# Kernel tuning notes

Hardware: AMD Instinct MI355X
Metric: run time of the kernel (lower is better)

Reference implementation:

```python
import jax, jax.numpy as jnp
import numpy as np

M, K, N, G = 4096, 4096, 4096, 128


def setup_inputs() -> dict:
    key = jax.random.key(0)
    k1, k2, k3 = jax.random.split(key, 3)
    a = jax.random.normal(k1, (M, K), dtype=jnp.float16)
    # 4-bit unsigned quantized weights, values in [0, 16)
    w_q = jax.random.randint(k2, (K, N), 0, 16, dtype=jnp.int32)
    # group-wise scales: one per (k-group, n); small magnitude keeps fp16 output in range
    scale = jax.random.uniform(k3, (K // G, N), dtype=jnp.float16, minval=0.001, maxval=0.02)
    return {"a": a, "w_q": w_q, "scale": scale, "group_size": G}


def reference(a, w_q, scale, group_size):
    # Dequantize: w[k, n] = w_q[k, n] * scale[k // group_size, n]
    scale_full = jnp.repeat(scale, group_size, axis=0)  # [K, N]
    w = w_q.astype(a.dtype) * scale_full                # fp16 dequantized weight
    out = jnp.matmul(a, w, preferred_element_type=jnp.float32)
    return out.astype(jnp.float16)
```

## Files before the change

kernel.cpp:

```cpp
#include <hip/hip_runtime.h>
#include <hip/hip_fp16.h>

#define MDIM 4096
#define NDIM 4096
#define KDIM 4096
#define NT 256
#define WBLK 4096

typedef _Float16 f16x8 __attribute__((ext_vector_type(8)));
typedef float f32x4 __attribute__((ext_vector_type(4)));
typedef unsigned int u32;
typedef unsigned short u16;

__device__ inline __half2 as_half2(u32 u) { return __builtin_bit_cast(__half2, u); }
__device__ inline u32 as_u32(__half2 h) { return __builtin_bit_cast(u32, h); }
__device__ inline u32 pkrtz(float a, float b) {
  return __builtin_bit_cast(u32, __builtin_amdgcn_cvt_pkrtz(a, b));
}

__device__ inline void load16_to_lds(const void* g, void* l) {
  __builtin_amdgcn_global_load_lds(
      (__attribute__((address_space(1))) const u32*)g,
      (__attribute__((address_space(3))) u32*)l,
      16, 0, 0);
}

template <int VM>
__device__ __forceinline__ void wait_vmcnt() {
  if constexpr (VM == 8)
    asm volatile("s_waitcnt vmcnt(8)" ::: "memory");
  else if constexpr (VM == 4)
    asm volatile("s_waitcnt vmcnt(4)" ::: "memory");
  else
    asm volatile("s_waitcnt vmcnt(0)" ::: "memory");
}

__global__ __launch_bounds__(NT) void prep(const float* __restrict__ A,
                                           _Float16* __restrict__ A16,
                                           const int* __restrict__ Wq,
                                           const float* __restrict__ Sc,
                                           _Float16* __restrict__ Wt) {
  __shared__ u32 Lt[64 * 33];
  const int tid = threadIdx.x;

  if (blockIdx.x >= WBLK) {
    const size_t b = blockIdx.x - WBLK;
    const size_t base = (b * NT + tid) * 8;
    const float4 f0 = *(const float4*)(A + base);
    const float4 f1 = *(const float4*)(A + base + 4);
    u32 pk[4];
    pk[0] = pkrtz(f0.x, f0.y);
    pk[1] = pkrtz(f0.z, f0.w);
    pk[2] = pkrtz(f1.x, f1.y);
    pk[3] = pkrtz(f1.z, f1.w);
    *(uint4*)(A16 + base) = *(const uint4*)pk;
    return;
  }

  const int n0 = (blockIdx.x & 63) * 64;
  const int k0 = (blockIdx.x >> 6) * 64;
  const int g = k0 >> 7;

#pragma unroll
  for (int r = 0; r < 2; ++r) {
    const int idx = r * 256 + tid;
    const int kp = idx >> 4;
    const int col4 = (idx & 15) * 4;
    const int4 va = *(const int4*)(Wq + (size_t)(k0 + 2 * kp) * NDIM + n0 + col4);
    const int4 vb = *(const int4*)(Wq + (size_t)(k0 + 2 * kp + 1) * NDIM + n0 + col4);
    const float4 s = *(const float4*)(Sc + (size_t)g * NDIM + n0 + col4);
    const float sf[4] = {s.x, s.y, s.z, s.w};
    const int av[4] = {va.x, va.y, va.z, va.w};
    const int bv[4] = {vb.x, vb.y, vb.z, vb.w};
#pragma unroll
    for (int i = 0; i < 4; ++i) {
      const __half hs = __float2half(sf[i]);
      const __half2 s2 = __half2half2(hs);
      const __half2 nb = __half2half2(__hmul(hs, __float2half(-1024.0f)));
      const u32 u = (u32)av[i] | ((u32)bv[i] << 16) | 0x64006400u;
      Lt[(size_t)(col4 + i) * 33 + kp] = as_u32(__hfma2(as_half2(u), s2, nb));
    }
  }
  __syncthreads();

#pragma unroll
  for (int r = 0; r < 2; ++r) {
    const int idx = r * 256 + tid;
    const int n = idx >> 3;
    const int k2c = (idx & 7) * 4;
    u32 v[4];
#pragma unroll
    for (int j = 0; j < 4; ++j) v[j] = Lt[(size_t)n * 33 + k2c + j];
    *(uint4*)(Wt + (size_t)(n0 + n) * KDIM + k0 + k2c * 2) = *(const uint4*)v;
  }
}

__global__ __launch_bounds__(512, 2) void gemm_f16(const _Float16* __restrict__ A16,
                                                   const _Float16* __restrict__ Wt,
                                                   float* __restrict__ C) {
  __shared__ __align__(16) _Float16 As[4 * 256 * 32];
  __shared__ __align__(16) _Float16 Bs[4 * 256 * 32];

  const int tid = threadIdx.x;
  const int bx = blockIdx.x & 15;
  const int by = blockIdx.x >> 4;
  const int m_base = by * 256;
  const int n_base = bx * 256;

  const int wave = tid >> 6;
  const int lane = tid & 63;
  const int l15 = lane & 15;
  const int quad = lane >> 4;
  const int mq = wave >> 2;
  const int nq = wave & 3;
  const int gq = (l15 >> 1) & 3;
  const int pchunk = quad ^ gq;

  f32x4 acc[8][4];
#pragma unroll
  for (int i = 0; i < 8; ++i)
#pragma unroll
    for (int j = 0; j < 4; ++j) acc[i][j] = (f32x4)0.0f;

  auto stage = [&](int p) {
    const int T = p >> 1;
    const int h = p & 1;
    const int s = p & 3;
    const size_t kof = (size_t)T * 64 + (size_t)h * 32;
#pragma unroll
    for (int L = 0; L < 2; ++L) {
      const int cc = L * 512 + tid;
      const int row = cc >> 2;
      const int lch = (cc & 3) ^ ((row >> 1) & 3);
      load16_to_lds(A16 + (size_t)(m_base + row) * KDIM + kof + lch * 8,
                    (char*)As + (size_t)s * 16384 + (size_t)cc * 16);
    }
#pragma unroll
    for (int L = 0; L < 2; ++L) {
      const int cc = L * 512 + tid;
      const int row = cc >> 2;
      const int lch = (cc & 3) ^ ((row >> 1) & 3);
      load16_to_lds(Wt + (size_t)(n_base + row) * KDIM + kof + lch * 8,
                    (char*)Bs + (size_t)s * 16384 + (size_t)cc * 16);
    }
  };

  auto phase_body = [&](int p, bool dostage) {
    __builtin_amdgcn_s_barrier();
    asm volatile("" ::: "memory");
    const int s = p & 3;
    const _Float16* Ab = (const _Float16*)((const char*)As + (size_t)s * 16384);
    const _Float16* Bb = (const _Float16*)((const char*)Bs + (size_t)s * 16384);
    f16x8 af[8], bf[4];
#pragma unroll
    for (int i = 0; i < 8; ++i) {
      const int row = mq * 128 + i * 16 + l15;
      af[i] = *(const f16x8*)(Ab + (size_t)row * 32 + pchunk * 8);
    }
#pragma unroll
    for (int j = 0; j < 4; ++j) {
      const int row = nq * 64 + j * 16 + l15;
      bf[j] = *(const f16x8*)(Bb + (size_t)row * 32 + pchunk * 8);
    }
    if (dostage) stage(p + 3);
    asm volatile("s_waitcnt lgkmcnt(0)" ::: "memory");
    __builtin_amdgcn_sched_barrier(0);
    __builtin_amdgcn_s_setprio(1);
#pragma unroll
    for (int i = 0; i < 8; ++i)
#pragma unroll
      for (int j = 0; j < 4; ++j)
        acc[i][j] = __builtin_amdgcn_mfma_f32_16x16x32_f16(af[i], bf[j],
                                                           acc[i][j], 0, 0, 0);
    __builtin_amdgcn_s_setprio(0);
  };

  stage(0);
  stage(1);
  stage(2);

  for (int p = 0; p < 125; ++p) {
    wait_vmcnt<8>();
    phase_body(p, true);
  }
  wait_vmcnt<8>();
  phase_body(125, false);
  wait_vmcnt<4>();
  phase_body(126, false);
  wait_vmcnt<0>();
  phase_body(127, false);

#pragma unroll
  for (int i = 0; i < 8; ++i) {
#pragma unroll
    for (int j = 0; j < 4; ++j) {
      const int col = n_base + nq * 64 + j * 16 + l15;
#pragma unroll
      for (int r = 0; r < 4; ++r) {
        const int row = m_base + mq * 128 + i * 16 + quad * 4 + r;
        C[(size_t)row * NDIM + col] = __half2float(__float2half(acc[i][j][r]));
      }
    }
  }
}

#define STR 72
__global__ __launch_bounds__(NT) void qgemm_fused(
    const float* __restrict__ A, const int* __restrict__ Wq,
    const float* __restrict__ Sc, float* __restrict__ C) {
  __shared__ __align__(16) _Float16 As[128 * STR];
  __shared__ __align__(16) _Float16 Bs[128 * STR];
  const int tid = threadIdx.x;
  const int bx = blockIdx.x & 31, by = blockIdx.x >> 5;
  const int m_base = by * 128, n_base = bx * 128;
  const int wave = tid >> 6, lane = tid & 63;
  const int l15 = lane & 15, quad = lane >> 4;
  const int wm = (wave & 1) * 64, wn = (wave >> 1) * 64;
  const int bn_local = tid & 127, bk_half = (tid >> 7) * 8;
  const int gn = n_base + bn_local;
  f32x4 acc[4][4];
#pragma unroll
  for (int i = 0; i < 4; ++i)
#pragma unroll
    for (int j = 0; j < 4; ++j) acc[i][j] = (f32x4)0.0f;
  for (int kt = 0; kt < KDIM / 64; ++kt) {
    const int k0 = kt * 64;
    __syncthreads();
#pragma unroll
    for (int i = 0; i < 8; ++i) {
      const int c = i * 256 + tid;
      const int row = c >> 4, col4 = (c & 15) * 4;
      const float4 f = *(const float4*)(A + (size_t)(m_base + row) * KDIM + k0 + col4);
      u32 pk[2];
      pk[0] = pkrtz(f.x, f.y);
      pk[1] = pkrtz(f.z, f.w);
      *(uint2*)&As[(size_t)row * STR + col4] = *(const uint2*)pk;
    }
    {
      const __half hs = __float2half(Sc[(size_t)(k0 >> 7) * NDIM + gn]);
      const __half2 s2 = __half2half2(hs);
      const __half2 nb2 = __half2half2(__hmul(hs, __float2half(-1024.0f)));
#pragma unroll
      for (int it = 0; it < 4; ++it) {
        const int k = bk_half + it * 16;
        u32 v[8];
#pragma unroll
        for (int j = 0; j < 8; ++j)
          v[j] = (u32)Wq[(size_t)(k0 + k + j) * NDIM + gn];
        u32 pk[4];
#pragma unroll
        for (int p = 0; p < 4; ++p) {
          u32 u = v[2 * p] | (v[2 * p + 1] << 16) | 0x64006400u;
          pk[p] = as_u32(__hfma2(as_half2(u), s2, nb2));
        }
        *(uint4*)&Bs[(size_t)bn_local * STR + k] = *(const uint4*)pk;
      }
    }
    __syncthreads();
#pragma unroll
    for (int ks = 0; ks < 64; ks += 32) {
      f16x8 af[4], bf[4];
#pragma unroll
      for (int i = 0; i < 4; ++i)
        af[i] = *(const f16x8*)&As[(size_t)(wm + i * 16 + l15) * STR + ks + quad * 8];
#pragma unroll
      for (int j = 0; j < 4; ++j)
        bf[j] = *(const f16x8*)&Bs[(size_t)(wn + j * 16 + l15) * STR + ks + quad * 8];
#pragma unroll
      for (int i = 0; i < 4; ++i)
#pragma unroll
        for (int j = 0; j < 4; ++j)
          acc[i][j] = __builtin_amdgcn_mfma_f32_16x16x32_f16(af[i], bf[j],
                                                             acc[i][j], 0, 0, 0);
    }
  }
#pragma unroll
  for (int i = 0; i < 4; ++i)
#pragma unroll
    for (int j = 0; j < 4; ++j) {
      const int col = n_base + wn + j * 16 + l15;
#pragma unroll
      for (int r = 0; r < 4; ++r) {
        const int row = m_base + wm + i * 16 + quad * 4 + r;
        C[(size_t)row * NDIM + col] = __half2float(__float2half(acc[i][j][r]));
      }
    }
}

extern "C" void kernel_launch(void* const* d_in, const int* in_sizes, int n_in,
                              void* d_out, int out_size, void* d_ws, size_t ws_size,
                              hipStream_t stream) {
  const float* a = (const float*)d_in[0];
  const int* wq = (const int*)d_in[1];
  const float* sc = (const float*)d_in[2];
  float* out = (float*)d_out;

  const size_t a16_bytes = (size_t)MDIM * KDIM * 2;
  const size_t wt_bytes = (size_t)NDIM * KDIM * 2;

  if (ws_size >= a16_bytes + wt_bytes) {
    _Float16* a16 = (_Float16*)d_ws;
    _Float16* wt = (_Float16*)((char*)d_ws + a16_bytes);
    const int a_blocks = (MDIM * KDIM) / (NT * 8);
    prep<<<WBLK + a_blocks, NT, 0, stream>>>(a, a16, wq, sc, wt);
    gemm_f16<<<(MDIM / 256) * (NDIM / 256), 512, 0, stream>>>(a16, wt, out);
  } else {
    qgemm_fused<<<(MDIM / 128) * (NDIM / 128), NT, 0, stream>>>(a, wq, sc, out);
  }
}
```

Measured before the change: 286.0 us.

## Split each k-phase into two half-tile MFMA pieces with interleaved A/B staging

Each 32-wide k phase is restructured into two halves. The first half reads 4 A fragments plus all B fragments, stages the next A tile, then runs 16 MFMAs. The second half reads the other 4 A fragments, stages the next B tile, then runs the remaining MFMAs. Barriers now sit between the halves and after the vmcnt wait, so global-to-LDS issue and LDS reads interleave more finely with MFMA work and fewer fragment registers are live at once. The cost is extra barriers per phase.

```diff
diff --git a/kernel.cpp b/kernel.cpp
--- a/kernel.cpp
+++ b/kernel.cpp
@@ -33,6 +33,16 @@
     asm volatile("s_waitcnt vmcnt(4)" ::: "memory");
   else
     asm volatile("s_waitcnt vmcnt(0)" ::: "memory");
+}
+
+__device__ __forceinline__ void wait_lgkm0_fence() {
+  asm volatile("s_waitcnt lgkmcnt(0)" ::: "memory");
+  __builtin_amdgcn_sched_barrier(0);
+}
+
+__device__ __forceinline__ void barrier_fence() {
+  __builtin_amdgcn_s_barrier();
+  asm volatile("" ::: "memory");
 }
 
 __global__ __launch_bounds__(NT) void prep(const float* __restrict__ A,
@@ -122,11 +132,9 @@
 #pragma unroll
     for (int j = 0; j < 4; ++j) acc[i][j] = (f32x4)0.0f;
 
-  auto stage = [&](int p) {
-    const int T = p >> 1;
-    const int h = p & 1;
-    const int s = p & 3;
-    const size_t kof = (size_t)T * 64 + (size_t)h * 32;
+  auto stageA = [&](int q) {
+    const size_t kof = (size_t)q * 32;
+    const int s = q & 3;
 #pragma unroll
     for (int L = 0; L < 2; ++L) {
       const int cc = L * 512 + tid;
@@ -135,6 +143,10 @@
       load16_to_lds(A16 + (size_t)(m_base + row) * KDIM + kof + lch * 8,
                     (char*)As + (size_t)s * 16384 + (size_t)cc * 16);
     }
+  };
+  auto stageB = [&](int q) {
+    const size_t kof = (size_t)q * 32;
+    const int s = q & 3;
 #pragma unroll
     for (int L = 0; L < 2; ++L) {
       const int cc = L * 512 + tid;
@@ -145,15 +157,14 @@
     }
   };
 
-  auto phase_body = [&](int p, bool dostage) {
-    __builtin_amdgcn_s_barrier();
-    asm volatile("" ::: "memory");
+  auto piece = [&](int p, bool dostage) {
     const int s = p & 3;
     const _Float16* Ab = (const _Float16*)((const char*)As + (size_t)s * 16384);
     const _Float16* Bb = (const _Float16*)((const char*)Bs + (size_t)s * 16384);
     f16x8 af[8], bf[4];
-#pragma unroll
-    for (int i = 0; i < 8; ++i) {
+
+#pragma unroll
+    for (int i = 0; i < 4; ++i) {
       const int row = mq * 128 + i * 16 + l15;
       af[i] = *(const f16x8*)(Ab + (size_t)row * 32 + pchunk * 8);
     }
@@ -162,12 +173,30 @@
       const int row = nq * 64 + j * 16 + l15;
       bf[j] = *(const f16x8*)(Bb + (size_t)row * 32 + pchunk * 8);
     }
-    if (dostage) stage(p + 3);
-    asm volatile("s_waitcnt lgkmcnt(0)" ::: "memory");
-    __builtin_amdgcn_sched_barrier(0);
+    if (dostage) stageA(p + 3);
+    barrier_fence();
+    wait_lgkm0_fence();
     __builtin_amdgcn_s_setprio(1);
 #pragma unroll
-    for (int i = 0; i < 8; ++i)
+    for (int i = 0; i < 4; ++i)
+#pragma unroll
+      for (int j = 0; j < 4; ++j)
+        acc[i][j] = __builtin_amdgcn_mfma_f32_16x16x32_f16(af[i], bf[j],
+                                                           acc[i][j], 0, 0, 0);
+    __builtin_amdgcn_s_setprio(0);
+    barrier_fence();
+
+#pragma unroll
+    for (int i = 4; i < 8; ++i) {
+      const int row = mq * 128 + i * 16 + l15;
+      af[i] = *(const f16x8*)(Ab + (size_t)row * 32 + pchunk * 8);
+    }
+    if (dostage) stageB(p + 3);
+    barrier_fence();
+    wait_lgkm0_fence();
+    __builtin_amdgcn_s_setprio(1);
+#pragma unroll
+    for (int i = 4; i < 8; ++i)
 #pragma unroll
       for (int j = 0; j < 4; ++j)
         acc[i][j] = __builtin_amdgcn_mfma_f32_16x16x32_f16(af[i], bf[j],
@@ -175,20 +204,24 @@
     __builtin_amdgcn_s_setprio(0);
   };
 
-  stage(0);
-  stage(1);
-  stage(2);
+  stageA(0); stageB(0);
+  stageA(1); stageB(1);
+  stageA(2); stageB(2);
+  wait_vmcnt<8>();
+  barrier_fence();
 
   for (int p = 0; p < 125; ++p) {
+    piece(p, true);
     wait_vmcnt<8>();
-    phase_body(p, true);
-  }
-  wait_vmcnt<8>();
-  phase_body(125, false);
+    barrier_fence();
+  }
+  piece(125, false);
   wait_vmcnt<4>();
-  phase_body(126, false);
+  barrier_fence();
+  piece(126, false);
   wait_vmcnt<0>();
-  phase_body(127, false);
+  barrier_fence();
+  piece(127, false);
 
 #pragma unroll
   for (int i = 0; i < 8; ++i) {
```

After: 291.5 us. Within noise of the previous version (+1.9%).

## Shrink GEMM tile to 128x256 with 256 threads and 3-stage pipeline

Applied to the files above, without the earlier changes.

The f16 GEMM moves from 256x256 tiles with 512 threads and a 4-deep LDS ring to 128x256 tiles with 256 threads and a 3-deep ring. Grid size doubles to 512 blocks, and the per-block LDS footprint shrinks so more blocks can be resident per CU. The aim is better CU load balance and occupancy. In exchange, each loaded A/B element is reused less and the prefetch distance is shorter, which may expose more memory latency.

```diff
diff --git a/kernel.cpp b/kernel.cpp
--- a/kernel.cpp
+++ b/kernel.cpp
@@ -27,10 +27,8 @@
 
 template <int VM>
 __device__ __forceinline__ void wait_vmcnt() {
-  if constexpr (VM == 8)
-    asm volatile("s_waitcnt vmcnt(8)" ::: "memory");
-  else if constexpr (VM == 4)
-    asm volatile("s_waitcnt vmcnt(4)" ::: "memory");
+  if constexpr (VM == 6)
+    asm volatile("s_waitcnt vmcnt(6)" ::: "memory");
   else
     asm volatile("s_waitcnt vmcnt(0)" ::: "memory");
 }
@@ -95,24 +93,22 @@
   }
 }
 
-__global__ __launch_bounds__(512, 2) void gemm_f16(const _Float16* __restrict__ A16,
-                                                   const _Float16* __restrict__ Wt,
-                                                   float* __restrict__ C) {
-  __shared__ __align__(16) _Float16 As[4 * 256 * 32];
-  __shared__ __align__(16) _Float16 Bs[4 * 256 * 32];
+__global__ __launch_bounds__(NT, 2) void gemm_f16(const _Float16* __restrict__ A16,
+                                                  const _Float16* __restrict__ Wt,
+                                                  float* __restrict__ C) {
+  __shared__ __align__(16) _Float16 As[3 * 128 * 32];
+  __shared__ __align__(16) _Float16 Bs[3 * 256 * 32];
 
   const int tid = threadIdx.x;
   const int bx = blockIdx.x & 15;
   const int by = blockIdx.x >> 4;
-  const int m_base = by * 256;
+  const int m_base = by * 128;
   const int n_base = bx * 256;
 
-  const int wave = tid >> 6;
   const int lane = tid & 63;
   const int l15 = lane & 15;
   const int quad = lane >> 4;
-  const int mq = wave >> 2;
-  const int nq = wave & 3;
+  const int nq = tid >> 6;
   const int gq = (l15 >> 1) & 3;
   const int pchunk = quad ^ gq;
 
@@ -122,39 +118,35 @@
 #pragma unroll
     for (int j = 0; j < 4; ++j) acc[i][j] = (f32x4)0.0f;
 
-  auto stage = [&](int p) {
-    const int T = p >> 1;
-    const int h = p & 1;
-    const int s = p & 3;
-    const size_t kof = (size_t)T * 64 + (size_t)h * 32;
+  auto stage = [&](int q, int sq) {
+    const size_t kof = (size_t)q * 32;
 #pragma unroll
     for (int L = 0; L < 2; ++L) {
-      const int cc = L * 512 + tid;
+      const int cc = L * 256 + tid;
       const int row = cc >> 2;
       const int lch = (cc & 3) ^ ((row >> 1) & 3);
       load16_to_lds(A16 + (size_t)(m_base + row) * KDIM + kof + lch * 8,
-                    (char*)As + (size_t)s * 16384 + (size_t)cc * 16);
-    }
-#pragma unroll
-    for (int L = 0; L < 2; ++L) {
-      const int cc = L * 512 + tid;
+                    (char*)As + (size_t)sq * 8192 + (size_t)cc * 16);
+    }
+#pragma unroll
+    for (int L = 0; L < 4; ++L) {
+      const int cc = L * 256 + tid;
       const int row = cc >> 2;
       const int lch = (cc & 3) ^ ((row >> 1) & 3);
       load16_to_lds(Wt + (size_t)(n_base + row) * KDIM + kof + lch * 8,
-                    (char*)Bs + (size_t)s * 16384 + (size_t)cc * 16);
+                    (char*)Bs + (size_t)sq * 16384 + (size_t)cc * 16);
     }
   };
 
-  auto phase_body = [&](int p, bool dostage) {
+  auto phase_body = [&](int p, int s, bool dostage) {
     __builtin_amdgcn_s_barrier();
     asm volatile("" ::: "memory");
-    const int s = p & 3;
-    const _Float16* Ab = (const _Float16*)((const char*)As + (size_t)s * 16384);
+    const _Float16* Ab = (const _Float16*)((const char*)As + (size_t)s * 8192);
     const _Float16* Bb = (const _Float16*)((const char*)Bs + (size_t)s * 16384);
     f16x8 af[8], bf[4];
 #pragma unroll
     for (int i = 0; i < 8; ++i) {
-      const int row = mq * 128 + i * 16 + l15;
+      const int row = i * 16 + l15;
       af[i] = *(const f16x8*)(Ab + (size_t)row * 32 + pchunk * 8);
     }
 #pragma unroll
@@ -162,7 +154,11 @@
       const int row = nq * 64 + j * 16 + l15;
       bf[j] = *(const f16x8*)(Bb + (size_t)row * 32 + pchunk * 8);
     }
-    if (dostage) stage(p + 3);
+    if (dostage) {
+      int s2 = s + 2;
+      if (s2 >= 3) s2 -= 3;
+      stage(p + 2, s2);
+    }
     asm volatile("s_waitcnt lgkmcnt(0)" ::: "memory");
     __builtin_amdgcn_sched_barrier(0);
     __builtin_amdgcn_s_setprio(1);
@@ -175,20 +171,20 @@
     __builtin_amdgcn_s_setprio(0);
   };
 
-  stage(0);
-  stage(1);
-  stage(2);
-
-  for (int p = 0; p < 125; ++p) {
-    wait_vmcnt<8>();
-    phase_body(p, true);
-  }
-  wait_vmcnt<8>();
-  phase_body(125, false);
-  wait_vmcnt<4>();
-  phase_body(126, false);
+  stage(0, 0);
+  stage(1, 1);
+
+  int s = 0;
+  for (int p = 0; p < 126; ++p) {
+    wait_vmcnt<6>();
+    phase_body(p, s, true);
+    if (++s == 3) s = 0;
+  }
+  wait_vmcnt<6>();
+  phase_body(126, s, false);
+  if (++s == 3) s = 0;
   wait_vmcnt<0>();
-  phase_body(127, false);
+  phase_body(127, s, false);
 
 #pragma unroll
   for (int i = 0; i < 8; ++i) {
@@ -197,7 +193,7 @@
       const int col = n_base + nq * 64 + j * 16 + l15;
 #pragma unroll
       for (int r = 0; r < 4; ++r) {
-        const int row = m_base + mq * 128 + i * 16 + quad * 4 + r;
+        const int row = m_base + i * 16 + quad * 4 + r;
         C[(size_t)row * NDIM + col] = __half2float(__float2half(acc[i][j][r]));
       }
     }
@@ -303,7 +299,7 @@
     _Float16* wt = (_Float16*)((char*)d_ws + a16_bytes);
     const int a_blocks = (MDIM * KDIM) / (NT * 8);
     prep<<<WBLK + a_blocks, NT, 0, stream>>>(a, a16, wq, sc, wt);
-    gemm_f16<<<(MDIM / 256) * (NDIM / 256), 512, 0, stream>>>(a16, wt, out);
+    gemm_f16<<<(MDIM / 128) * (NDIM / 256), NT, 0, stream>>>(a16, wt, out);
   } else {
     qgemm_fused<<<(MDIM / 128) * (NDIM / 128), NT, 0, stream>>>(a, wq, sc, out);
   }
```

Measured after the change: 297.7 us. +4.1%, slower.

## Load B fragments directly from global into registers and remap blocks per XCD

Applied to the files above, without the earlier changes.

B tiles now go straight from global memory into per-wave register fragments, double-buffered across phases, and no longer pass through LDS. Only A is staged through LDS, with a pipeline depth of two instead of three, and the vmcnt waits are adjusted to match. LDS use is halved and the launch-bounds occupancy hint of 2 is dropped. Block indices are also remapped so that blocks on the same XCD share N-columns, for better L2 reuse. The costs are redundant global loads of B across the two M-waves, higher register pressure, and shallower A prefetch.

```diff
diff --git a/kernel.cpp b/kernel.cpp
--- a/kernel.cpp
+++ b/kernel.cpp
@@ -27,10 +27,8 @@
 
 template <int VM>
 __device__ __forceinline__ void wait_vmcnt() {
-  if constexpr (VM == 8)
-    asm volatile("s_waitcnt vmcnt(8)" ::: "memory");
-  else if constexpr (VM == 4)
-    asm volatile("s_waitcnt vmcnt(4)" ::: "memory");
+  if constexpr (VM == 6)
+    asm volatile("s_waitcnt vmcnt(6)" ::: "memory");
   else
     asm volatile("s_waitcnt vmcnt(0)" ::: "memory");
 }
@@ -95,15 +93,17 @@
   }
 }
 
-__global__ __launch_bounds__(512, 2) void gemm_f16(const _Float16* __restrict__ A16,
-                                                   const _Float16* __restrict__ Wt,
-                                                   float* __restrict__ C) {
+__global__ __launch_bounds__(512) void gemm_f16(const _Float16* __restrict__ A16,
+                                                const _Float16* __restrict__ Wt,
+                                                float* __restrict__ C) {
   __shared__ __align__(16) _Float16 As[4 * 256 * 32];
-  __shared__ __align__(16) _Float16 Bs[4 * 256 * 32];
 
   const int tid = threadIdx.x;
-  const int bx = blockIdx.x & 15;
-  const int by = blockIdx.x >> 4;
+  const int g = blockIdx.x;
+  const int xcd = g & 7;
+  const int i5 = g >> 3;
+  const int bx = xcd * 2 + (i5 & 1);
+  const int by = i5 >> 1;
   const int m_base = by * 256;
   const int n_base = bx * 256;
 
@@ -122,11 +122,19 @@
 #pragma unroll
     for (int j = 0; j < 4; ++j) acc[i][j] = (f32x4)0.0f;
 
-  auto stage = [&](int p) {
-    const int T = p >> 1;
-    const int h = p & 1;
-    const int s = p & 3;
-    const size_t kof = (size_t)T * 64 + (size_t)h * 32;
+  const _Float16* const wt_base =
+      Wt + (size_t)(n_base + nq * 64 + l15) * KDIM + quad * 8;
+
+  auto loadB = [&](int q, f16x8(&bf)[4]) {
+    const _Float16* src = wt_base + (size_t)q * 32;
+#pragma unroll
+    for (int j = 0; j < 4; ++j)
+      bf[j] = *(const f16x8*)(src + (size_t)(j * 16) * KDIM);
+  };
+
+  auto stageA = [&](int q) {
+    const size_t kof = (size_t)q * 32;
+    const int s = q & 3;
 #pragma unroll
     for (int L = 0; L < 2; ++L) {
       const int cc = L * 512 + tid;
@@ -135,34 +143,20 @@
       load16_to_lds(A16 + (size_t)(m_base + row) * KDIM + kof + lch * 8,
                     (char*)As + (size_t)s * 16384 + (size_t)cc * 16);
     }
-#pragma unroll
-    for (int L = 0; L < 2; ++L) {
-      const int cc = L * 512 + tid;
-      const int row = cc >> 2;
-      const int lch = (cc & 3) ^ ((row >> 1) & 3);
-      load16_to_lds(Wt + (size_t)(n_base + row) * KDIM + kof + lch * 8,
-                    (char*)Bs + (size_t)s * 16384 + (size_t)cc * 16);
-    }
   };
 
-  auto phase_body = [&](int p, bool dostage) {
+  auto phase_body = [&](int p, f16x8(&bf)[4], bool dostage) {
     __builtin_amdgcn_s_barrier();
     asm volatile("" ::: "memory");
     const int s = p & 3;
     const _Float16* Ab = (const _Float16*)((const char*)As + (size_t)s * 16384);
-    const _Float16* Bb = (const _Float16*)((const char*)Bs + (size_t)s * 16384);
-    f16x8 af[8], bf[4];
+    f16x8 af[8];
 #pragma unroll
     for (int i = 0; i < 8; ++i) {
       const int row = mq * 128 + i * 16 + l15;
       af[i] = *(const f16x8*)(Ab + (size_t)row * 32 + pchunk * 8);
     }
-#pragma unroll
-    for (int j = 0; j < 4; ++j) {
-      const int row = nq * 64 + j * 16 + l15;
-      bf[j] = *(const f16x8*)(Bb + (size_t)row * 32 + pchunk * 8);
-    }
-    if (dostage) stage(p + 3);
+    if (dostage) stageA(p + 2);
     asm volatile("s_waitcnt lgkmcnt(0)" ::: "memory");
     __builtin_amdgcn_sched_barrier(0);
     __builtin_amdgcn_s_setprio(1);
@@ -173,22 +167,26 @@
         acc[i][j] = __builtin_amdgcn_mfma_f32_16x16x32_f16(af[i], bf[j],
                                                            acc[i][j], 0, 0, 0);
     __builtin_amdgcn_s_setprio(0);
+    if (dostage) loadB(p + 2, bf);
   };
 
-  stage(0);
-  stage(1);
-  stage(2);
-
-  for (int p = 0; p < 125; ++p) {
-    wait_vmcnt<8>();
-    phase_body(p, true);
-  }
-  wait_vmcnt<8>();
-  phase_body(125, false);
-  wait_vmcnt<4>();
-  phase_body(126, false);
+  f16x8 bfA[4], bfB[4];
+
+  stageA(0);
+  loadB(0, bfA);
+  stageA(1);
+  loadB(1, bfB);
+
+  for (int p = 0; p < 126; p += 2) {
+    wait_vmcnt<6>();
+    phase_body(p, bfA, true);
+    wait_vmcnt<6>();
+    phase_body(p + 1, bfB, true);
+  }
+  wait_vmcnt<6>();
+  phase_body(126, bfA, false);
   wait_vmcnt<0>();
-  phase_body(127, false);
+  phase_body(127, bfB, false);
 
 #pragma unroll
   for (int i = 0; i < 8; ++i) {
```

New measurement: 342.6 us. +19.8%, slower.
